# Optimization experiments

Hardware: AMD Instinct MI355X
Metric: run time of the kernel (lower is better)

## Reference

```python
import jax, jax.numpy as jnp
import numpy as np

B, H, W = 32, 56, 56
C_IN, C_OUT, GROUPS, K = 256, 256, 32, 3
EPS = 1e-5


def setup_inputs() -> dict:
    key = jax.random.key(0)
    k1, k2 = jax.random.split(key, 2)
    x = jax.random.normal(k1, (B, H, W, C_IN), dtype=jnp.float32)
    # HWIO grouped-conv kernel: I = C_IN // GROUPS = 8; equivalent to the
    # concatenation of the 32 per-group [3,3,8,8] Conv2d kernels along O.
    w = jax.random.normal(k2, (K, K, C_IN // GROUPS, C_OUT), dtype=jnp.float32) * 0.05
    b = jnp.zeros((C_OUT,), dtype=jnp.float32)
    gamma = jnp.ones((C_OUT,), dtype=jnp.float32)
    beta = jnp.zeros((C_OUT,), dtype=jnp.float32)
    return {"x": x, "w": w, "b": b, "gamma": gamma, "beta": beta}


def reference(x, w, b, gamma, beta):
    # Grouped conv: same math as tf.split -> per-group Conv2d -> tf.concat,
    # expressed as one native grouped convolution (feature_group_count).
    y = jax.lax.conv_general_dilated(
        x, w,
        window_strides=(1, 1),
        padding="SAME",
        dimension_numbers=("NHWC", "HWIO", "NHWC"),
        feature_group_count=GROUPS,
    ) + b  # [B,H,W,C_OUT]
    # BatchNorm (training forward: batch statistics over N,H,W per channel)
    mean = jnp.mean(y, axis=(0, 1, 2))
    var = jnp.var(y, axis=(0, 1, 2))
    y = (y - mean) * jax.lax.rsqrt(var + EPS) * gamma + beta
    # Act('relu')
    return jax.nn.relu(y)
```

## Files before the change

kernel.cpp:

```cpp
#include <hip/hip_runtime.h>
#include <hip/hip_bf16.h>

#define BB 32
#define HH 56
#define WW 56
#define CC 256
#define NPIX (BB*HH*WW)
#define EPS 1e-5f

typedef short bf16x8 __attribute__((ext_vector_type(8)));
typedef float f32x4  __attribute__((ext_vector_type(4)));
typedef unsigned int u32;

#define COLB 272
#define ROWB (30*COLB)

__device__ __forceinline__ unsigned short f2bf(float f) {
    __hip_bfloat16 h = __float2bfloat16(f);
    return *reinterpret_cast<unsigned short*>(&h);
}


__global__ __launch_bounds__(512, 4) void k1_conv(
    const float* __restrict__ x, const float* __restrict__ wgt,
    __hip_bfloat16* __restrict__ y, float* __restrict__ stats)
{
    __shared__ __align__(16) unsigned char xs[6*ROWB];
    __shared__ float bsum[128], bsq[128];

    const int cq   = blockIdx.x & 1;
    const int chh  = blockIdx.x >> 1;
    const int hb   = blockIdx.y;
    const int b    = blockIdx.z;
    const int t    = threadIdx.x;
    const int lane = t & 63;
    const int w    = t >> 6;
    const int r0   = hb*4, c0 = cq*28;
    const int chbase = chh*128;

    if (t < 128) { bsum[t] = 0.f; bsq[t] = 0.f; }

    #pragma unroll
    for (int jc = 0; jc < 2; ++jc) {
        float4 a[3], c[3];
        int so[3], iv[3];
        #pragma unroll
        for (int j = 0; j < 3; ++j) {
            const int i   = (jc*3 + j)*512 + t;
            const int oct = i & 15;
            const int pix = i >> 4;
            const int row = pix / 30;
            const int col = pix - row*30;
            const int gh  = r0 - 1 + row;
            const int gw  = c0 - 1 + col;
            so[j] = row*ROWB + col*COLB + oct*16;
            iv[j] = (i < 2880);
            const bool ok = iv[j] && ((unsigned)gh < HH) && ((unsigned)gw < WW);
            const float* p = x + ((size_t)((b*HH + gh)*WW + gw))*CC + chbase + oct*8;
            a[j] = ok ? *(const float4*)p       : make_float4(0.f,0.f,0.f,0.f);
            c[j] = ok ? *(const float4*)(p + 4) : make_float4(0.f,0.f,0.f,0.f);
        }
        #pragma unroll
        for (int j = 0; j < 3; ++j) {
            if (iv[j]) {
                u32 a0 = __float_as_uint(a[j].x) + 0x8000u;
                u32 a1 = __float_as_uint(a[j].y) + 0x8000u;
                u32 a2 = __float_as_uint(a[j].z) + 0x8000u;
                u32 a3 = __float_as_uint(a[j].w) + 0x8000u;
                u32 a4 = __float_as_uint(c[j].x) + 0x8000u;
                u32 a5 = __float_as_uint(c[j].y) + 0x8000u;
                u32 a6 = __float_as_uint(c[j].z) + 0x8000u;
                u32 a7 = __float_as_uint(c[j].w) + 0x8000u;
                uint4 pk;
                pk.x = __builtin_amdgcn_perm(a1, a0, 0x07060302u);
                pk.y = __builtin_amdgcn_perm(a3, a2, 0x07060302u);
                pk.z = __builtin_amdgcn_perm(a5, a4, 0x07060302u);
                pk.w = __builtin_amdgcn_perm(a7, a6, 0x07060302u);
                *(uint4*)(xs + so[j]) = pk;
            }
        }
    }

    const int n = lane & 15;
    const int q = lane >> 4;
    bf16x8 bfrag[5];
    #pragma unroll
    for (int s = 0; s < 5; ++s) {
        const int o  = s*4 + q;
        const int g  = (o >= 10);
        const int tp = o - g*10;
        const int tp0 = (tp == 9) ? 0 : tp;
        const bool val = (tp < 9) && ((n >> 3) == g);
        const float* wp = wgt + tp0*8*CC + chbase + w*16 + n;
        #pragma unroll
        for (int ci = 0; ci < 8; ++ci) {
            float f = val ? wp[ci*CC] : 0.f;
            bfrag[s][ci] = (short)f2bf(f);
        }
    }

    const int pr = (lane & 15) >> 2;
    const int pc = lane & 3;
    int aoff[5];
    #pragma unroll
    for (int s = 0; s < 5; ++s) {
        const int o  = s*4 + q;
        const int g  = (o >= 10);
        int tp = o - g*10;
        if (tp == 9) tp = 0;
        const int dh = tp / 3, dw = tp - dh*3;
        aoff[s] = (pr + dh)*ROWB + (pc + dw)*COLB + (2*w + g)*16;
    }

    __syncthreads();

    const int cb = chbase + w*16 + n;
    float lsum = 0.f, lsq = 0.f;

    #pragma unroll
    for (int ct = 0; ct < 7; ++ct) {
        f32x4 acc = {0.f, 0.f, 0.f, 0.f};
        #pragma unroll
        for (int s = 0; s < 5; ++s) {
            bf16x8 af = *(const bf16x8*)(xs + aoff[s] + ct*(4*COLB));
            acc = __builtin_amdgcn_mfma_f32_16x16x32_bf16(af, bfrag[s], acc, 0, 0, 0);
        }
        const int h = r0 + q;
        const size_t base = ((size_t)((b*HH + h)*WW + c0 + ct*4))*CC + cb;
        #pragma unroll
        for (int i = 0; i < 4; ++i) {
            float vv = acc[i];
            y[base + (size_t)i*CC] = __float2bfloat16(vv);
            lsum += vv;
            lsq  += vv * vv;
        }
    }

    atomicAdd(&bsum[w*16 + n], lsum);
    atomicAdd(&bsq[w*16 + n],  lsq);
    __syncthreads();
    if (t < 128) {
        atomicAdd(&stats[chbase + t],       bsum[t]);
        atomicAdd(&stats[256 + chbase + t], bsq[t]);
    }
}

__global__ __launch_bounds__(256) void k3_norm(
    const __hip_bfloat16* __restrict__ y, const float* __restrict__ stats,
    const float* __restrict__ gamma, const float* __restrict__ beta,
    float* __restrict__ out)
{
    __shared__ float lss[512];
    const int t = threadIdx.x;
    {
        const float inv_n = 1.f / (float)NPIX;
        float mean = stats[t] * inv_n;
        float var  = stats[256 + t] * inv_n - mean * mean;
        float sc   = gamma[t] * rsqrtf(var + EPS);
        lss[t]       = sc;
        lss[256 + t] = beta[t] - mean * sc;
    }
    __syncthreads();

    const int oct = t & 31;
    const int pr  = t >> 5;
    const int c0  = oct * 8;

    float4 sc0 = *(const float4*)(lss + c0);
    float4 sc1 = *(const float4*)(lss + c0 + 4);
    float4 sh0 = *(const float4*)(lss + 256 + c0);
    float4 sh1 = *(const float4*)(lss + 256 + c0 + 4);

    const uint4* yv = (const uint4*)y;
    const int px0 = blockIdx.x * 16 + pr;

    uint4 d[2];
    #pragma unroll
    for (int i = 0; i < 2; ++i)
        d[i] = yv[(size_t)(px0 + i*8)*32 + oct];

    #pragma unroll
    for (int i = 0; i < 2; ++i) {
        const int px = px0 + i*8;
        float f0 = __uint_as_float((d[i].x & 0xffffu) << 16);
        float f1 = __uint_as_float(d[i].x & 0xffff0000u);
        float f2 = __uint_as_float((d[i].y & 0xffffu) << 16);
        float f3 = __uint_as_float(d[i].y & 0xffff0000u);
        float f4 = __uint_as_float((d[i].z & 0xffffu) << 16);
        float f5 = __uint_as_float(d[i].z & 0xffff0000u);
        float f6 = __uint_as_float((d[i].w & 0xffffu) << 16);
        float f7 = __uint_as_float(d[i].w & 0xffff0000u);

        f32x4 o0, o1;
        o0[0] = fmaxf(0.f, f0 * sc0.x + sh0.x);
        o0[1] = fmaxf(0.f, f1 * sc0.y + sh0.y);
        o0[2] = fmaxf(0.f, f2 * sc0.z + sh0.z);
        o0[3] = fmaxf(0.f, f3 * sc0.w + sh0.w);
        o1[0] = fmaxf(0.f, f4 * sc1.x + sh1.x);
        o1[1] = fmaxf(0.f, f5 * sc1.y + sh1.y);
        o1[2] = fmaxf(0.f, f6 * sc1.z + sh1.z);
        o1[3] = fmaxf(0.f, f7 * sc1.w + sh1.w);

        f32x4* op = (f32x4*)out + (size_t)px*64 + oct*2;
        __builtin_nontemporal_store(o0, op);
        __builtin_nontemporal_store(o1, op + 1);
    }
}

extern "C" void kernel_launch(void* const* d_in, const int* in_sizes, int n_in,
                              void* d_out, int out_size, void* d_ws, size_t ws_size,
                              hipStream_t stream) {
    const float* x     = (const float*)d_in[0];
    const float* wgt   = (const float*)d_in[1];
    const float* gamma = (const float*)d_in[3];
    const float* beta  = (const float*)d_in[4];
    float* out = (float*)d_out;

    float* stats = (float*)d_ws;
    __hip_bfloat16* y = (__hip_bfloat16*)((char*)d_ws + 4096);

    hipMemsetAsync(stats, 0, 2048, stream);
    k1_conv<<<dim3(4, 14, BB), 512, 0, stream>>>(x, wgt, y, stats);
    k3_norm<<<NPIX/16, 256, 0, stream>>>(y, stats, gamma, beta, out);
}
```

Baseline: 250.4 us.

## Recompute grouped conv in a fused output pass instead of storing bf16 intermediate

Drops the bf16 intermediate tensor. The first kernel now only computes the per-channel sum and sum of squares, and a second kernel reruns the convolution with the batch-norm scale/shift and ReLU fused in. This removes the intermediate write and re-read (about 50 MB of traffic) at the cost of reading x twice and doing the MFMA work twice. The MFMA operands are swapped so each lane holds 4 consecutive channels, which allows vectorized float4 output stores and a shuffle-based stats reduction in place of per-thread shared atomics.

```diff
diff --git a/kernel.cpp b/kernel.cpp
--- a/kernel.cpp
+++ b/kernel.cpp
@@ -21,25 +21,10 @@
 }
 
 
-__global__ __launch_bounds__(512, 4) void k1_conv(
-    const float* __restrict__ x, const float* __restrict__ wgt,
-    __hip_bfloat16* __restrict__ y, float* __restrict__ stats)
-{
-    __shared__ __align__(16) unsigned char xs[6*ROWB];
-    __shared__ float bsum[128], bsq[128];
-
-    const int cq   = blockIdx.x & 1;
-    const int chh  = blockIdx.x >> 1;
-    const int hb   = blockIdx.y;
-    const int b    = blockIdx.z;
-    const int t    = threadIdx.x;
-    const int lane = t & 63;
-    const int w    = t >> 6;
-    const int r0   = hb*4, c0 = cq*28;
-    const int chbase = chh*128;
-
-    if (t < 128) { bsum[t] = 0.f; bsq[t] = 0.f; }
-
+
+__device__ __forceinline__ void stage_tile(const float* __restrict__ x,
+    unsigned char* xs, int b, int r0, int c0, int chbase, int t)
+{
     #pragma unroll
     for (int jc = 0; jc < 2; ++jc) {
         float4 a[3], c[3];
@@ -80,64 +65,97 @@
             }
         }
     }
-
-    const int n = lane & 15;
+}
+
+__device__ __forceinline__ void gather_w(const float* __restrict__ wgt,
+    int chbase, int w, int lane, bf16x8* wfrag)
+{
+    const int m = lane & 15;
     const int q = lane >> 4;
-    bf16x8 bfrag[5];
     #pragma unroll
     for (int s = 0; s < 5; ++s) {
         const int o  = s*4 + q;
         const int g  = (o >= 10);
         const int tp = o - g*10;
         const int tp0 = (tp == 9) ? 0 : tp;
-        const bool val = (tp < 9) && ((n >> 3) == g);
-        const float* wp = wgt + tp0*8*CC + chbase + w*16 + n;
+        const bool val = (tp < 9) && ((m >> 3) == g);
+        const float* wp = wgt + tp0*8*CC + chbase + w*16 + m;
         #pragma unroll
         for (int ci = 0; ci < 8; ++ci) {
             float f = val ? wp[ci*CC] : 0.f;
-            bfrag[s][ci] = (short)f2bf(f);
-        }
-    }
-
+            wfrag[s][ci] = (short)f2bf(f);
+        }
+    }
+}
+
+__device__ __forceinline__ void calc_aoff(int lane, int w, int* aoff)
+{
+    const int q  = lane >> 4;
     const int pr = (lane & 15) >> 2;
     const int pc = lane & 3;
-    int aoff[5];
     #pragma unroll
     for (int s = 0; s < 5; ++s) {
-        const int o  = s*4 + q;
-        const int g  = (o >= 10);
+        const int o = s*4 + q;
+        const int g = (o >= 10);
         int tp = o - g*10;
         if (tp == 9) tp = 0;
         const int dh = tp / 3, dw = tp - dh*3;
         aoff[s] = (pr + dh)*ROWB + (pc + dw)*COLB + (2*w + g)*16;
     }
+}
+
+__global__ __launch_bounds__(512) void k1a_stats(
+    const float* __restrict__ x, const float* __restrict__ wgt,
+    float* __restrict__ stats)
+{
+    __shared__ __align__(16) unsigned char xs[6*ROWB];
+    __shared__ __align__(16) float bsum[128], bsq[128];
+
+    const int cq   = blockIdx.x & 1;
+    const int chh  = blockIdx.x >> 1;
+    const int hb   = blockIdx.y;
+    const int b    = blockIdx.z;
+    const int t    = threadIdx.x;
+    const int lane = t & 63;
+    const int w    = t >> 6;
+    const int r0   = hb*4, c0 = cq*28;
+    const int chbase = chh*128;
+
+    stage_tile(x, xs, b, r0, c0, chbase, t);
+
+    bf16x8 wfrag[5];
+    gather_w(wgt, chbase, w, lane, wfrag);
+    int aoff[5];
+    calc_aoff(lane, w, aoff);
 
     __syncthreads();
 
-    const int cb = chbase + w*16 + n;
-    float lsum = 0.f, lsq = 0.f;
-
+    f32x4 s1 = {0.f,0.f,0.f,0.f}, s2 = {0.f,0.f,0.f,0.f};
     #pragma unroll
     for (int ct = 0; ct < 7; ++ct) {
-        f32x4 acc = {0.f, 0.f, 0.f, 0.f};
+        f32x4 acc = {0.f,0.f,0.f,0.f};
         #pragma unroll
         for (int s = 0; s < 5; ++s) {
-            bf16x8 af = *(const bf16x8*)(xs + aoff[s] + ct*(4*COLB));
-            acc = __builtin_amdgcn_mfma_f32_16x16x32_bf16(af, bfrag[s], acc, 0, 0, 0);
-        }
-        const int h = r0 + q;
-        const size_t base = ((size_t)((b*HH + h)*WW + c0 + ct*4))*CC + cb;
+            bf16x8 xf = *(const bf16x8*)(xs + aoff[s] + ct*(4*COLB));
+            acc = __builtin_amdgcn_mfma_f32_16x16x32_bf16(wfrag[s], xf, acc, 0, 0, 0);
+        }
+        #pragma unroll
+        for (int i = 0; i < 4; ++i) { s1[i] += acc[i]; s2[i] += acc[i]*acc[i]; }
+    }
+
+    #pragma unroll
+    for (int d = 1; d < 16; d <<= 1) {
         #pragma unroll
         for (int i = 0; i < 4; ++i) {
-            float vv = acc[i];
-            y[base + (size_t)i*CC] = __float2bfloat16(vv);
-            lsum += vv;
-            lsq  += vv * vv;
-        }
-    }
-
-    atomicAdd(&bsum[w*16 + n], lsum);
-    atomicAdd(&bsq[w*16 + n],  lsq);
+            s1[i] += __shfl_xor(s1[i], d);
+            s2[i] += __shfl_xor(s2[i], d);
+        }
+    }
+    const int q = lane >> 4;
+    if ((lane & 15) == 0) {
+        *(f32x4*)&bsum[w*16 + q*4] = s1;
+        *(f32x4*)&bsq[w*16 + q*4]  = s2;
+    }
     __syncthreads();
     if (t < 128) {
         atomicAdd(&stats[chbase + t],       bsum[t]);
@@ -145,65 +163,65 @@
     }
 }
 
-__global__ __launch_bounds__(256) void k3_norm(
-    const __hip_bfloat16* __restrict__ y, const float* __restrict__ stats,
-    const float* __restrict__ gamma, const float* __restrict__ beta,
-    float* __restrict__ out)
-{
-    __shared__ float lss[512];
-    const int t = threadIdx.x;
-    {
-        const float inv_n = 1.f / (float)NPIX;
-        float mean = stats[t] * inv_n;
-        float var  = stats[256 + t] * inv_n - mean * mean;
-        float sc   = gamma[t] * rsqrtf(var + EPS);
-        lss[t]       = sc;
-        lss[256 + t] = beta[t] - mean * sc;
-    }
+__global__ __launch_bounds__(512) void k1b_out(
+    const float* __restrict__ x, const float* __restrict__ wgt,
+    const float* __restrict__ stats, const float* __restrict__ gamma,
+    const float* __restrict__ beta, float* __restrict__ out)
+{
+    __shared__ __align__(16) unsigned char xs[6*ROWB];
+
+    const int cq   = blockIdx.x & 1;
+    const int chh  = blockIdx.x >> 1;
+    const int hb   = blockIdx.y;
+    const int b    = blockIdx.z;
+    const int t    = threadIdx.x;
+    const int lane = t & 63;
+    const int w    = t >> 6;
+    const int r0   = hb*4, c0 = cq*28;
+    const int chbase = chh*128;
+
+    stage_tile(x, xs, b, r0, c0, chbase, t);
+
+    bf16x8 wfrag[5];
+    gather_w(wgt, chbase, w, lane, wfrag);
+    int aoff[5];
+    calc_aoff(lane, w, aoff);
+
+    const int q  = lane >> 4;
+    const int c4 = chbase + w*16 + q*4;
+    f32x4 sum = *(const f32x4*)(stats + c4);
+    f32x4 ssq = *(const f32x4*)(stats + 256 + c4);
+    f32x4 gm  = *(const f32x4*)(gamma + c4);
+    f32x4 bt  = *(const f32x4*)(beta + c4);
+    f32x4 sc, sh;
+    const float inv_n = 1.f / (float)NPIX;
+    #pragma unroll
+    for (int i = 0; i < 4; ++i) {
+        float mean = sum[i] * inv_n;
+        float var  = ssq[i] * inv_n - mean*mean;
+        sc[i] = gm[i] * rsqrtf(var + EPS);
+        sh[i] = bt[i] - mean * sc[i];
+    }
+
     __syncthreads();
 
-    const int oct = t & 31;
-    const int pr  = t >> 5;
-    const int c0  = oct * 8;
-
-    float4 sc0 = *(const float4*)(lss + c0);
-    float4 sc1 = *(const float4*)(lss + c0 + 4);
-    float4 sh0 = *(const float4*)(lss + 256 + c0);
-    float4 sh1 = *(const float4*)(lss + 256 + c0 + 4);
-
-    const uint4* yv = (const uint4*)y;
-    const int px0 = blockIdx.x * 16 + pr;
-
-    uint4 d[2];
-    #pragma unroll
-    for (int i = 0; i < 2; ++i)
-        d[i] = yv[(size_t)(px0 + i*8)*32 + oct];
-
-    #pragma unroll
-    for (int i = 0; i < 2; ++i) {
-        const int px = px0 + i*8;
-        float f0 = __uint_as_float((d[i].x & 0xffffu) << 16);
-        float f1 = __uint_as_float(d[i].x & 0xffff0000u);
-        float f2 = __uint_as_float((d[i].y & 0xffffu) << 16);
-        float f3 = __uint_as_float(d[i].y & 0xffff0000u);
-        float f4 = __uint_as_float((d[i].z & 0xffffu) << 16);
-        float f5 = __uint_as_float(d[i].z & 0xffff0000u);
-        float f6 = __uint_as_float((d[i].w & 0xffffu) << 16);
-        float f7 = __uint_as_float(d[i].w & 0xffff0000u);
-
-        f32x4 o0, o1;
-        o0[0] = fmaxf(0.f, f0 * sc0.x + sh0.x);
-        o0[1] = fmaxf(0.f, f1 * sc0.y + sh0.y);
-        o0[2] = fmaxf(0.f, f2 * sc0.z + sh0.z);
-        o0[3] = fmaxf(0.f, f3 * sc0.w + sh0.w);
-        o1[0] = fmaxf(0.f, f4 * sc1.x + sh1.x);
-        o1[1] = fmaxf(0.f, f5 * sc1.y + sh1.y);
-        o1[2] = fmaxf(0.f, f6 * sc1.z + sh1.z);
-        o1[3] = fmaxf(0.f, f7 * sc1.w + sh1.w);
-
-        f32x4* op = (f32x4*)out + (size_t)px*64 + oct*2;
-        __builtin_nontemporal_store(o0, op);
-        __builtin_nontemporal_store(o1, op + 1);
+    const int p  = lane & 15;
+    const int h  = r0 + (p >> 2);
+    const int wc0 = c0 + (p & 3);
+    #pragma unroll
+    for (int ct = 0; ct < 7; ++ct) {
+        f32x4 acc = {0.f,0.f,0.f,0.f};
+        #pragma unroll
+        for (int s = 0; s < 5; ++s) {
+            bf16x8 xf = *(const bf16x8*)(xs + aoff[s] + ct*(4*COLB));
+            acc = __builtin_amdgcn_mfma_f32_16x16x32_bf16(wfrag[s], xf, acc, 0, 0, 0);
+        }
+        f32x4 o;
+        #pragma unroll
+        for (int i = 0; i < 4; ++i)
+            o[i] = fmaxf(0.f, acc[i]*sc[i] + sh[i]);
+        f32x4* op = (f32x4*)(out + ((size_t)((b*HH + h)*WW + wc0 + ct*4))*CC + c4);
+        __builtin_nontemporal_store(o, op);
     }
 }
 
@@ -217,9 +235,8 @@
     float* out = (float*)d_out;
 
     float* stats = (float*)d_ws;
-    __hip_bfloat16* y = (__hip_bfloat16*)((char*)d_ws + 4096);
 
     hipMemsetAsync(stats, 0, 2048, stream);
-    k1_conv<<<dim3(4, 14, BB), 512, 0, stream>>>(x, wgt, y, stats);
-    k3_norm<<<NPIX/16, 256, 0, stream>>>(y, stats, gamma, beta, out);
-}
+    k1a_stats<<<dim3(4, 14, BB), 512, 0, stream>>>(x, wgt, stats);
+    k1b_out<<<dim3(4, 14, BB), 512, 0, stream>>>(x, wgt, stats, gamma, beta, out);
+}
```

After: 287.7 us. 14.9% more time.
